# Kernel tuning notes

Measured on AMD Instinct MI355X. Metric: run time of the kernel, lower is better.

Reference implementation:

```python
import jax, jax.numpy as jnp
import numpy as np

B, C, H, W = 16, 128, 48, 48
C4 = C // 4
N = H * W
BN_EPS = 1e-5


def conv_bn_relu(x, w, gamma, beta, mean, var):
    # 1x1 conv (no bias) as channel contraction, then eval-mode BatchNorm, then ReLU
    y = jnp.einsum('bchw,oc->bohw', x, w)
    scale = gamma / jnp.sqrt(var + BN_EPS)
    y = y * scale[None, :, None, None] + (beta - mean * scale)[None, :, None, None]
    return jax.nn.relu(y)


def setup_inputs() -> dict:
    key = jax.random.key(0)
    ks = jax.random.split(key, 16)
    inp = {
        'x_en': jax.random.normal(ks[0], (B, C, H, W), dtype=jnp.float32),
        'x_de': jax.random.normal(ks[1], (B, C, H, W), dtype=jnp.float32),
        'x_cat': jax.random.normal(ks[2], (B, 2 * C, H, W), dtype=jnp.float32),
        # Get_KQ: Conv2d(C -> C/4, 1x1, no bias) + BN(C/4) (shared for K and Q)
        'w_kq': jax.random.normal(ks[3], (C4, C), dtype=jnp.float32) * 0.05,
        'kq_gamma': jax.random.normal(ks[4], (C4,), dtype=jnp.float32) * 0.1 + 1.0,
        'kq_beta': jax.random.normal(ks[5], (C4,), dtype=jnp.float32) * 0.1,
        'kq_mean': jax.random.normal(ks[6], (C4,), dtype=jnp.float32) * 0.1,
        'kq_var': jax.random.uniform(ks[7], (C4,), dtype=jnp.float32) + 0.5,
        # Get_V: Conv2d(C -> C, 1x1, no bias) + BN(C)
        'w_v': jax.random.normal(ks[8], (C, C), dtype=jnp.float32) * 0.05,
        'v_gamma': jax.random.normal(ks[9], (C,), dtype=jnp.float32) * 0.1 + 1.0,
        'v_beta': jax.random.normal(ks[10], (C,), dtype=jnp.float32) * 0.1,
        'v_mean': jax.random.normal(ks[11], (C,), dtype=jnp.float32) * 0.1,
        'v_var': jax.random.uniform(ks[12], (C,), dtype=jnp.float32) + 0.5,
        # reduce_channels: Conv2d(2C -> C, 1x1, no bias) + BN(C)
        'w_red': jax.random.normal(ks[13], (C, 2 * C), dtype=jnp.float32) * 0.05,
        'red_gamma': jax.random.normal(ks[14], (C,), dtype=jnp.float32) * 0.1 + 1.0,
        'red_beta': jax.random.normal(ks[15], (C,), dtype=jnp.float32) * 0.1,
        'red_mean': jax.random.normal(jax.random.fold_in(key, 100), (C,), dtype=jnp.float32) * 0.1,
        'red_var': jax.random.uniform(jax.random.fold_in(key, 101), (C,), dtype=jnp.float32) + 0.5,
    }
    return inp


def reference(x_en, x_de, x_cat,
              w_kq, kq_gamma, kq_beta, kq_mean, kq_var,
              w_v, v_gamma, v_beta, v_mean, v_var,
              w_red, red_gamma, red_beta, red_mean, red_var):
    Kf = conv_bn_relu(x_en, w_kq, kq_gamma, kq_beta, kq_mean, kq_var).reshape(B, C4, N)
    Qf = conv_bn_relu(x_de, w_kq, kq_gamma, kq_beta, kq_mean, kq_var).reshape(B, C4, N)
    # KQ[b, n, m] = sum_k K[b, k, n] * Q[b, k, m]  -> [B, N, N]
    KQ = jnp.einsum('bkn,bkm->bnm', Kf, Qf)
    # GLOBAL softmax over the flattened N*N map (per batch), not per row
    A = jax.nn.softmax(KQ.reshape(B, N * N), axis=1).reshape(B, N, N)
    x = conv_bn_relu(x_cat, w_red, red_gamma, red_beta, red_mean, red_var)
    V = conv_bn_relu(x, w_v, v_gamma, v_beta, v_mean, v_var).reshape(B, C, N)
    # FeatureMap[b, c, n] = sum_m V[b, c, m] * A[b, n, m]
    feat = jnp.einsum('bcm,bnm->bcn', V, A).reshape(B, C, H, W)
    return jnp.concatenate([x, feat], axis=1)
```

## Files before the change

### kernel.cpp

```cpp
#include <hip/hip_runtime.h>
#include <math.h>

#define C    128
#define C4   32
#define NN   2304
#define BN_EPS 1e-5f
#define NEG_INF -3.402823466e38f
#define LOG2E 1.4426950408889634f

typedef short bf16x8 __attribute__((ext_vector_type(8)));
typedef float f32x4 __attribute__((ext_vector_type(4)));

#define SOFT_BARRIER() asm volatile("s_waitcnt lgkmcnt(0)\n\ts_barrier" ::: "memory")

__device__ inline unsigned short f2bf(float f) {
    unsigned int u = __float_as_uint(f);
    u += 0x7fffu + ((u >> 16) & 1u);
    return (unsigned short)(u >> 16);
}

__device__ inline unsigned int pk2bf(float a, float b) {
#if __has_builtin(__builtin_amdgcn_cvt_pk_bf16_f32)
    typedef __bf16 bf2 __attribute__((ext_vector_type(2)));
    bf2 v = __builtin_amdgcn_cvt_pk_bf16_f32(a, b);
    return __builtin_bit_cast(unsigned int, v);
#else
    unsigned int ua = __float_as_uint(a); ua += 0x7fffu + ((ua >> 16) & 1u);
    unsigned int ub = __float_as_uint(b); ub += 0x7fffu + ((ub >> 16) & 1u);
    return __builtin_amdgcn_perm(ub, ua, 0x07060302u);
#endif
}

__device__ inline float fexp2(float x) {
#if __has_builtin(__builtin_amdgcn_exp2f)
    return __builtin_amdgcn_exp2f(x);
#else
    return __expf(x * 0.69314718055994531f);
#endif
}


__global__ __launch_bounds__(256) void k_wprep(
    const float* __restrict__ wkq, const float* __restrict__ kq_g,
    const float* __restrict__ kq_b, const float* __restrict__ kq_m,
    const float* __restrict__ kq_v,
    const float* __restrict__ wv, const float* __restrict__ v_g,
    const float* __restrict__ v_b, const float* __restrict__ v_m,
    const float* __restrict__ v_v,
    const float* __restrict__ wred, const float* __restrict__ red_g,
    const float* __restrict__ red_b, const float* __restrict__ red_m,
    const float* __restrict__ red_v,
    unsigned short* __restrict__ wkq_bf, unsigned short* __restrict__ wv_bf,
    unsigned short* __restrict__ wred_bf,
    float* __restrict__ kq_sh, float* __restrict__ v_sh, float* __restrict__ red_sh)
{
    const int t = blockIdx.x * 256 + threadIdx.x;
    if (t < 4096) {
        const int o = t >> 7;
        const float sc = kq_g[o] * rsqrtf(kq_v[o] + BN_EPS);
        wkq_bf[t] = f2bf(wkq[t] * sc);
        if ((t & 127) == 0) kq_sh[o] = kq_b[o] - kq_m[o] * sc;
    } else if (t < 4096 + 16384) {
        const int e = t - 4096;
        const int o = e >> 7;
        const float sc = v_g[o] * rsqrtf(v_v[o] + BN_EPS);
        wv_bf[e] = f2bf(wv[e] * sc);
        if ((e & 127) == 0) v_sh[o] = v_b[o] - v_m[o] * sc;
    } else if (t < 4096 + 16384 + 32768) {
        const int e = t - 20480;
        const int o = e >> 8;
        const float sc = red_g[o] * rsqrtf(red_v[o] + BN_EPS);
        wred_bf[e] = f2bf(wred[e] * sc);
        if ((e & 255) == 0) red_sh[o] = red_b[o] - red_m[o] * sc;
    }
}

__global__ __launch_bounds__(256) void k_kq(
    const float* __restrict__ x0, const float* __restrict__ x1,
    const unsigned short* __restrict__ wbf, const float* __restrict__ shift,
    unsigned short* __restrict__ Kt, unsigned short* __restrict__ Qt)
{
    constexpr int NTILE = 128, R = 8;
    __shared__ unsigned short Xs[NTILE][40];

    const int tid = threadIdx.x;
    const int w = tid >> 6, lane = tid & 63;
    const int quad = lane >> 4, l16 = lane & 15;
    const int b = blockIdx.y, n0 = blockIdx.x * NTILE;
    const int nbase = w * 32;

    const float* xin = (blockIdx.z ? x1 : x0) + (size_t)b * C * NN;
    const int p = tid & 15, g = tid >> 4;

    f32x4 acc[2][2];
#pragma unroll
    for (int mt = 0; mt < 2; mt++)
#pragma unroll
        for (int nt = 0; nt < 2; nt++) acc[mt][nt] = (f32x4){0.f, 0.f, 0.f, 0.f};

    for (int c0 = 0; c0 < C; c0 += 32) {
        __syncthreads();
        {
            const float* xr = xin + (size_t)(c0 + 2 * p) * NN + n0 + g * R;
            float av[R], bv[R];
#pragma unroll
            for (int i4 = 0; i4 < R; i4 += 4) {
                *(float4*)&av[i4] = *(const float4*)&xr[i4];
                *(float4*)&bv[i4] = *(const float4*)&xr[NN + i4];
            }
            unsigned int* Xw = (unsigned int*)Xs;
#pragma unroll
            for (int i = 0; i < R; i++)
                Xw[(g * R + i) * 20 + p] = pk2bf(av[i], bv[i]);
        }
        __syncthreads();
        bf16x8 af[2];
#pragma unroll
        for (int mt = 0; mt < 2; mt++)
            af[mt] = *(const bf16x8*)&wbf[(size_t)(mt * 16 + l16) * C + c0 + quad * 8];
#pragma unroll
        for (int nt = 0; nt < 2; nt++) {
            const bf16x8 bfr = *(const bf16x8*)&Xs[nbase + nt * 16 + l16][quad * 8];
#pragma unroll
            for (int mt = 0; mt < 2; mt++)
                acc[mt][nt] = __builtin_amdgcn_mfma_f32_16x16x32_bf16(af[mt], bfr, acc[mt][nt], 0, 0, 0);
        }
    }

    unsigned short* ob16 = blockIdx.z ? Qt : Kt;
    const float osc = blockIdx.z ? 1.f : LOG2E;
#pragma unroll
    for (int mt = 0; mt < 2; mt++)
#pragma unroll
        for (int nt = 0; nt < 2; nt++)
#pragma unroll
            for (int r = 0; r < 4; r++) {
                const int o = mt * 16 + quad * 4 + r;
                const int n = n0 + nbase + nt * 16 + l16;
                const float sh = shift[o];
                ob16[((size_t)b * NN + n) * 32 + o] =
                    f2bf(fmaxf(acc[mt][nt][r] + sh, 0.f) * osc);
            }
}

__global__ __launch_bounds__(256) void k_redv(
    const float* __restrict__ xcat,
    const unsigned short* __restrict__ wred_bf, const float* __restrict__ red_sh,
    const unsigned short* __restrict__ wv_bf,  const float* __restrict__ v_sh,
    float* __restrict__ out, unsigned short* __restrict__ Vf)
{
    __shared__ unsigned short Xs[48][40];
    __shared__ unsigned int   Xv[64 * 49];

    const int tid = threadIdx.x;
    const int w = tid >> 6, lane = tid & 63;
    const int quad = lane >> 4, l16 = lane & 15;
    const int b = blockIdx.y, n0 = blockIdx.x * 48;
    const float* xin = xcat + (size_t)b * 2 * C * NN;
    const int p = tid & 15, g = tid >> 4;

    f32x4 acc[2][3];
#pragma unroll
    for (int mt = 0; mt < 2; mt++)
#pragma unroll
        for (int nt = 0; nt < 3; nt++) acc[mt][nt] = (f32x4){0.f, 0.f, 0.f, 0.f};

    for (int c0 = 0; c0 < 2 * C; c0 += 32) {
        __syncthreads();
        if (g < 12) {
            const float* xr = xin + (size_t)(c0 + 2 * p) * NN + n0 + g * 4;
            float4 av = *(const float4*)&xr[0];
            float4 bv = *(const float4*)&xr[NN];
            unsigned int* Xw = (unsigned int*)Xs;
            Xw[(g * 4 + 0) * 20 + p] = pk2bf(av.x, bv.x);
            Xw[(g * 4 + 1) * 20 + p] = pk2bf(av.y, bv.y);
            Xw[(g * 4 + 2) * 20 + p] = pk2bf(av.z, bv.z);
            Xw[(g * 4 + 3) * 20 + p] = pk2bf(av.w, bv.w);
        }
        __syncthreads();
        bf16x8 af[2];
#pragma unroll
        for (int mt = 0; mt < 2; mt++)
            af[mt] = *(const bf16x8*)&wred_bf[(size_t)(w * 32 + mt * 16 + l16) * (2 * C) + c0 + quad * 8];
#pragma unroll
        for (int nt = 0; nt < 3; nt++) {
            const bf16x8 bfr = *(const bf16x8*)&Xs[nt * 16 + l16][quad * 8];
#pragma unroll
            for (int mt = 0; mt < 2; mt++)
                acc[mt][nt] = __builtin_amdgcn_mfma_f32_16x16x32_bf16(af[mt], bfr, acc[mt][nt], 0, 0, 0);
        }
    }

    {
        float* ob = out + (size_t)b * (2 * C * NN);
#pragma unroll
        for (int mt = 0; mt < 2; mt++) {
            float sh[4];
#pragma unroll
            for (int r = 0; r < 4; r++) sh[r] = red_sh[w * 32 + mt * 16 + quad * 4 + r];
#pragma unroll
            for (int nt = 0; nt < 3; nt++) {
                const int n = n0 + nt * 16 + l16;
                float v[4];
#pragma unroll
                for (int r = 0; r < 4; r++) {
                    const int o = w * 32 + mt * 16 + quad * 4 + r;
                    v[r] = fmaxf(acc[mt][nt][r] + sh[r], 0.f);
                    ob[(size_t)o * NN + n] = v[r];
                }
                const int op0 = 16 * w + mt * 8 + quad * 2;
                Xv[(op0 + 0) * 49 + nt * 16 + l16] = pk2bf(v[0], v[1]);
                Xv[(op0 + 1) * 49 + nt * 16 + l16] = pk2bf(v[2], v[3]);
            }
        }
    }
    SOFT_BARRIER();

    f32x4 vacc[2][3];
#pragma unroll
    for (int mt = 0; mt < 2; mt++)
#pragma unroll
        for (int nt = 0; nt < 3; nt++) vacc[mt][nt] = (f32x4){0.f, 0.f, 0.f, 0.f};

    for (int c0 = 0; c0 < C; c0 += 32) {
        bf16x8 af[2];
#pragma unroll
        for (int mt = 0; mt < 2; mt++)
            af[mt] = *(const bf16x8*)&wv_bf[(size_t)(w * 32 + mt * 16 + l16) * C + c0 + quad * 8];
#pragma unroll
        for (int nt = 0; nt < 3; nt++) {
            const int col = nt * 16 + l16;
            const int cp0 = c0 / 2 + quad * 4;
            uint4 u;
            u.x = Xv[(cp0 + 0) * 49 + col];
            u.y = Xv[(cp0 + 1) * 49 + col];
            u.z = Xv[(cp0 + 2) * 49 + col];
            u.w = Xv[(cp0 + 3) * 49 + col];
            const bf16x8 bfr = __builtin_bit_cast(bf16x8, u);
#pragma unroll
            for (int mt = 0; mt < 2; mt++)
                vacc[mt][nt] = __builtin_amdgcn_mfma_f32_16x16x32_bf16(af[mt], bfr, vacc[mt][nt], 0, 0, 0);
        }
    }

#pragma unroll
    for (int mt = 0; mt < 2; mt++) {
        float sh[4];
#pragma unroll
        for (int r = 0; r < 4; r++) sh[r] = v_sh[w * 32 + mt * 16 + quad * 4 + r];
#pragma unroll
        for (int nt = 0; nt < 3; nt++)
#pragma unroll
            for (int r = 0; r < 4; r++) {
                const int o = w * 32 + mt * 16 + quad * 4 + r;
                const int n = n0 + nt * 16 + l16;
                Vf[((size_t)b * C + o) * NN + n] = f2bf(fmaxf(vacc[mt][nt][r] + sh[r], 0.f));
            }
    }
}

__global__ __launch_bounds__(256) void k_stats(
    const unsigned short* __restrict__ Kt, const unsigned short* __restrict__ Qt,
    float* __restrict__ bmax, float* __restrict__ bsum)
{
    const int tid = threadIdx.x;
    const int w = tid >> 6, lane = tid & 63;
    const int quad = lane >> 4, l16 = lane & 15;
    const int b = blockIdx.z;
    const int n0 = blockIdx.x * 128, m0 = blockIdx.y * 128;
    const unsigned short* Kb = Kt + (size_t)b * NN * 32;
    const unsigned short* Qb = Qt + (size_t)b * NN * 32;

    bf16x8 kf[8], qf[2];
#pragma unroll
    for (int nt = 0; nt < 8; nt++)
        kf[nt] = *(const bf16x8*)&Kb[(size_t)(n0 + nt * 16 + l16) * 32 + quad * 8];
#pragma unroll
    for (int mt = 0; mt < 2; mt++)
        qf[mt] = *(const bf16x8*)&Qb[(size_t)(m0 + w * 32 + mt * 16 + l16) * 32 + quad * 8];

    f32x4 s[16];
#pragma unroll
    for (int mt = 0; mt < 2; mt++)
#pragma unroll
        for (int nt = 0; nt < 8; nt++) {
            f32x4 z = (f32x4){0.f, 0.f, 0.f, 0.f};
            s[mt * 8 + nt] = __builtin_amdgcn_mfma_f32_16x16x32_bf16(qf[mt], kf[nt], z, 0, 0, 0);
        }

    float lmax = NEG_INF;
#pragma unroll
    for (int i = 0; i < 16; i++)
        lmax = fmaxf(lmax, fmaxf(fmaxf(s[i][0], s[i][1]), fmaxf(s[i][2], s[i][3])));
    float lsum = 0.f;
#pragma unroll
    for (int i = 0; i < 16; i++)
        lsum += fexp2(s[i][0] - lmax) + fexp2(s[i][1] - lmax) +
                fexp2(s[i][2] - lmax) + fexp2(s[i][3] - lmax);

#pragma unroll
    for (int off = 32; off > 0; off >>= 1) {
        const float omax = __shfl_xor(lmax, off);
        const float osum = __shfl_xor(lsum, off);
        const float nmax = fmaxf(lmax, omax);
        lsum = lsum * fexp2(lmax - nmax) + osum * fexp2(omax - nmax);
        lmax = nmax;
    }
    __shared__ float smax[4], ssum[4];
    if (lane == 0) { smax[w] = lmax; ssum[w] = lsum; }
    __syncthreads();
    if (tid == 0) {
        float M = smax[0], S = ssum[0];
        for (int i = 1; i < 4; i++) {
            const float nmax = fmaxf(M, smax[i]);
            S = S * fexp2(M - nmax) + ssum[i] * fexp2(smax[i] - nmax);
            M = nmax;
        }
        const int idx = (b * 18 + blockIdx.y) * 18 + blockIdx.x;
        bmax[idx] = M;
        bsum[idx] = S;
    }
}

__global__ __launch_bounds__(256) void k_fin(
    const float* __restrict__ bmax, const float* __restrict__ bsum,
    float* __restrict__ Ms, float* __restrict__ Sinv)
{
    __shared__ float rmax[256], rsum[256];
    const int b = blockIdx.x, tid = threadIdx.x;
    float lmax = NEG_INF, lsum = 0.f;
    for (int i = tid; i < 324; i += 256) {
        const float m = bmax[b * 324 + i], s = bsum[b * 324 + i];
        const float nmax = fmaxf(lmax, m);
        lsum = lsum * fexp2(lmax - nmax) + s * fexp2(m - nmax);
        lmax = nmax;
    }
    rmax[tid] = lmax; rsum[tid] = lsum;
    __syncthreads();
    for (int st = 128; st > 0; st >>= 1) {
        if (tid < st) {
            const float m2 = rmax[tid + st], s2 = rsum[tid + st];
            const float nmax = fmaxf(rmax[tid], m2);
            rsum[tid] = rsum[tid] * fexp2(rmax[tid] - nmax) + s2 * fexp2(m2 - nmax);
            rmax[tid] = nmax;
        }
        __syncthreads();
    }
    if (tid == 0) { Ms[b] = rmax[0]; Sinv[b] = 1.f / rsum[0]; }
}

__global__ __launch_bounds__(256) void k_feat(
    const unsigned short* __restrict__ Kt, const unsigned short* __restrict__ Qt,
    const unsigned short* __restrict__ Vf, const float* __restrict__ Ms,
    const float* __restrict__ Sinv, float* __restrict__ out)
{
    __shared__ __align__(16) unsigned short Et[48][72];
    const int tid = threadIdx.x;
    const int w = tid >> 6, lane = tid & 63;
    const int quad = lane >> 4, l16 = lane & 15;
    const int b = blockIdx.y, n0 = blockIdx.x * 48;
    const unsigned short* Kb = Kt + (size_t)b * NN * 32;
    const unsigned short* Qb = Qt + (size_t)b * NN * 32;
    const unsigned short* Vb = Vf + (size_t)b * C * NN;
    const float M = Ms[b], Si = Sinv[b];

    bf16x8 kf[3];
#pragma unroll
    for (int nt = 0; nt < 3; nt++)
        kf[nt] = *(const bf16x8*)&Kb[(size_t)(n0 + nt * 16 + l16) * 32 + quad * 8];

    f32x4 acc[2][3];
#pragma unroll
    for (int i = 0; i < 2; i++)
#pragma unroll
        for (int j = 0; j < 3; j++) acc[i][j] = (f32x4){0.f, 0.f, 0.f, 0.f};

    bf16x8 qc = *(const bf16x8*)&Qb[(size_t)(w * 16 + l16) * 32 + quad * 8];
    bf16x8 vc[2][2];
#pragma unroll
    for (int ct = 0; ct < 2; ct++)
#pragma unroll
        for (int ks = 0; ks < 2; ks++)
            vc[ct][ks] = *(const bf16x8*)&Vb[(size_t)(w * 32 + ct * 16 + l16) * NN + ks * 32 + quad * 8];

    for (int m0 = 0; m0 < NN; m0 += 64) {
        f32x4 s[3];
#pragma unroll
        for (int nt = 0; nt < 3; nt++) {
            f32x4 z = (f32x4){0.f, 0.f, 0.f, 0.f};
            s[nt] = __builtin_amdgcn_mfma_f32_16x16x32_bf16(qc, kf[nt], z, 0, 0, 0);
        }
        const int m1 = (m0 + 64 < NN) ? m0 + 64 : 0;
        bf16x8 qn = *(const bf16x8*)&Qb[(size_t)(m1 + w * 16 + l16) * 32 + quad * 8];
        bf16x8 vn[2][2];
#pragma unroll
        for (int ct = 0; ct < 2; ct++)
#pragma unroll
            for (int ks = 0; ks < 2; ks++)
                vn[ct][ks] = *(const bf16x8*)&Vb[(size_t)(w * 32 + ct * 16 + l16) * NN + m1 + ks * 32 + quad * 8];

#pragma unroll
        for (int nt = 0; nt < 3; nt++) {
            const unsigned int u0 = pk2bf(fexp2(s[nt][0] - M), fexp2(s[nt][1] - M));
            const unsigned int u1 = pk2bf(fexp2(s[nt][2] - M), fexp2(s[nt][3] - M));
            *(uint2*)&Et[nt * 16 + l16][w * 16 + quad * 4] = make_uint2(u0, u1);
        }
        SOFT_BARRIER();
#pragma unroll
        for (int ks = 0; ks < 2; ks++) {
#pragma unroll
            for (int nt = 0; nt < 3; nt++) {
                const bf16x8 ef = *(const bf16x8*)&Et[nt * 16 + l16][ks * 32 + quad * 8];
                acc[0][nt] = __builtin_amdgcn_mfma_f32_16x16x32_bf16(vc[0][ks], ef, acc[0][nt], 0, 0, 0);
                acc[1][nt] = __builtin_amdgcn_mfma_f32_16x16x32_bf16(vc[1][ks], ef, acc[1][nt], 0, 0, 0);
            }
        }
        SOFT_BARRIER();
        qc = qn;
#pragma unroll
        for (int ct = 0; ct < 2; ct++)
#pragma unroll
            for (int ks = 0; ks < 2; ks++) vc[ct][ks] = vn[ct][ks];
    }

    float* ob = out + (size_t)b * 2 * C * NN + (size_t)C * NN + n0;
#pragma unroll
    for (int ct = 0; ct < 2; ct++)
#pragma unroll
        for (int nt = 0; nt < 3; nt++)
#pragma unroll
            for (int r = 0; r < 4; r++) {
                const int c = w * 32 + ct * 16 + quad * 4 + r;
                ob[(size_t)c * NN + nt * 16 + l16] = acc[ct][nt][r] * Si;
            }
}

extern "C" void kernel_launch(void* const* d_in, const int* in_sizes, int n_in,
                              void* d_out, int out_size, void* d_ws, size_t ws_size,
                              hipStream_t stream)
{
    const float* x_en   = (const float*)d_in[0];
    const float* x_de   = (const float*)d_in[1];
    const float* x_cat  = (const float*)d_in[2];
    const float* w_kq   = (const float*)d_in[3];
    const float* kq_g   = (const float*)d_in[4];
    const float* kq_b   = (const float*)d_in[5];
    const float* kq_m   = (const float*)d_in[6];
    const float* kq_v   = (const float*)d_in[7];
    const float* w_v    = (const float*)d_in[8];
    const float* v_g    = (const float*)d_in[9];
    const float* v_b    = (const float*)d_in[10];
    const float* v_m    = (const float*)d_in[11];
    const float* v_v    = (const float*)d_in[12];
    const float* w_red  = (const float*)d_in[13];
    const float* red_g  = (const float*)d_in[14];
    const float* red_b  = (const float*)d_in[15];
    const float* red_m  = (const float*)d_in[16];
    const float* red_v  = (const float*)d_in[17];

    unsigned short* Kt      = (unsigned short*)d_ws;
    unsigned short* Qt      = Kt + 1179648;
    unsigned short* Vf      = Qt + 1179648;
    unsigned short* wkq_bf  = Vf + 4718592;
    unsigned short* wv_bf   = wkq_bf + 4096;
    unsigned short* wred_bf = wv_bf + 16384;
    float* bmax = (float*)(wred_bf + 32768);
    float* bsum = bmax + 16 * 324;
    float* Ms   = bsum + 16 * 324;
    float* Sinv = Ms + 16;
    float* kq_sh  = Sinv + 16;
    float* v_sh   = kq_sh + 32;
    float* red_sh = v_sh + 128;
    float* out  = (float*)d_out;

    k_wprep<<<208, 256, 0, stream>>>(
        w_kq, kq_g, kq_b, kq_m, kq_v,
        w_v, v_g, v_b, v_m, v_v,
        w_red, red_g, red_b, red_m, red_v,
        wkq_bf, wv_bf, wred_bf, kq_sh, v_sh, red_sh);

    k_kq  <<<dim3(18, 16, 2), 256, 0, stream>>>(x_en, x_de, wkq_bf, kq_sh, Kt, Qt);
    k_redv<<<dim3(48, 16), 256, 0, stream>>>(x_cat, wred_bf, red_sh, wv_bf, v_sh, out, Vf);

    k_stats<<<dim3(18, 18, 16), 256, 0, stream>>>(Kt, Qt, bmax, bsum);
    k_fin  <<<16, 256, 0, stream>>>(bmax, bsum, Ms, Sinv);
    k_feat <<<dim3(48, 16), 256, 0, stream>>>(Kt, Qt, Vf, Ms, Sinv, out);
}
```

Baseline: 247.7 us.

## Double-buffer LDS tiles and software-pipeline loads in conv and attention kernels

The 1x1-conv kernels (k_kq, k_redv) now use two LDS buffers and prefetch the next channel slice into registers before writing the current one. This drops one barrier per iteration and overlaps global loads with MFMA work. k_feat double-buffers the exp-score tile: it computes scores and exponentials for the next 64-column chunk while the current chunk feeds the V·A MFMAs, so only one barrier per iteration remains. The cost is more LDS and register pressure, which could lower occupancy.

```diff
diff --git a/kernel.cpp b/kernel.cpp
--- a/kernel.cpp
+++ b/kernel.cpp
@@ -81,7 +81,7 @@
     unsigned short* __restrict__ Kt, unsigned short* __restrict__ Qt)
 {
     constexpr int NTILE = 128, R = 8;
-    __shared__ unsigned short Xs[NTILE][40];
+    __shared__ unsigned short Xs[2][NTILE][40];
 
     const int tid = threadIdx.x;
     const int w = tid >> 6, lane = tid & 63;
@@ -98,29 +98,41 @@
 #pragma unroll
         for (int nt = 0; nt < 2; nt++) acc[mt][nt] = (f32x4){0.f, 0.f, 0.f, 0.f};
 
-    for (int c0 = 0; c0 < C; c0 += 32) {
-        __syncthreads();
-        {
-            const float* xr = xin + (size_t)(c0 + 2 * p) * NN + n0 + g * R;
-            float av[R], bv[R];
+    const float* xrb = xin + n0 + g * R;
+    float av[R], bv[R];
+    {
+        const float* xr = xrb + (size_t)(2 * p) * NN;
+#pragma unroll
+        for (int i4 = 0; i4 < R; i4 += 4) {
+            *(float4*)&av[i4] = *(const float4*)&xr[i4];
+            *(float4*)&bv[i4] = *(const float4*)&xr[NN + i4];
+        }
+    }
+
+    for (int k = 0; k < 4; ++k) {
+        unsigned int uu[R];
+#pragma unroll
+        for (int i = 0; i < R; i++) uu[i] = pk2bf(av[i], bv[i]);
+        if (k < 3) {
+            const float* xr = xrb + (size_t)((k + 1) * 32 + 2 * p) * NN;
 #pragma unroll
             for (int i4 = 0; i4 < R; i4 += 4) {
                 *(float4*)&av[i4] = *(const float4*)&xr[i4];
                 *(float4*)&bv[i4] = *(const float4*)&xr[NN + i4];
             }
-            unsigned int* Xw = (unsigned int*)Xs;
-#pragma unroll
-            for (int i = 0; i < R; i++)
-                Xw[(g * R + i) * 20 + p] = pk2bf(av[i], bv[i]);
-        }
-        __syncthreads();
+        }
+        unsigned int* Xw = (unsigned int*)Xs[k & 1];
+#pragma unroll
+        for (int i = 0; i < R; i++)
+            Xw[(g * R + i) * 20 + p] = uu[i];
+        SOFT_BARRIER();
         bf16x8 af[2];
 #pragma unroll
         for (int mt = 0; mt < 2; mt++)
-            af[mt] = *(const bf16x8*)&wbf[(size_t)(mt * 16 + l16) * C + c0 + quad * 8];
+            af[mt] = *(const bf16x8*)&wbf[(size_t)(mt * 16 + l16) * C + k * 32 + quad * 8];
 #pragma unroll
         for (int nt = 0; nt < 2; nt++) {
-            const bf16x8 bfr = *(const bf16x8*)&Xs[nbase + nt * 16 + l16][quad * 8];
+            const bf16x8 bfr = *(const bf16x8*)&Xs[k & 1][nbase + nt * 16 + l16][quad * 8];
 #pragma unroll
             for (int mt = 0; mt < 2; mt++)
                 acc[mt][nt] = __builtin_amdgcn_mfma_f32_16x16x32_bf16(af[mt], bfr, acc[mt][nt], 0, 0, 0);
@@ -149,7 +161,7 @@
     const unsigned short* __restrict__ wv_bf,  const float* __restrict__ v_sh,
     float* __restrict__ out, unsigned short* __restrict__ Vf)
 {
-    __shared__ unsigned short Xs[48][40];
+    __shared__ unsigned short Xs[2][48][40];
     __shared__ unsigned int   Xv[64 * 49];
 
     const int tid = threadIdx.x;
@@ -165,26 +177,38 @@
 #pragma unroll
         for (int nt = 0; nt < 3; nt++) acc[mt][nt] = (f32x4){0.f, 0.f, 0.f, 0.f};
 
-    for (int c0 = 0; c0 < 2 * C; c0 += 32) {
-        __syncthreads();
+    float4 av, bv;
+    if (g < 12) {
+        const float* xr = xin + (size_t)(2 * p) * NN + n0 + g * 4;
+        av = *(const float4*)&xr[0];
+        bv = *(const float4*)&xr[NN];
+    }
+
+    for (int k = 0; k < 8; ++k) {
         if (g < 12) {
-            const float* xr = xin + (size_t)(c0 + 2 * p) * NN + n0 + g * 4;
-            float4 av = *(const float4*)&xr[0];
-            float4 bv = *(const float4*)&xr[NN];
-            unsigned int* Xw = (unsigned int*)Xs;
-            Xw[(g * 4 + 0) * 20 + p] = pk2bf(av.x, bv.x);
-            Xw[(g * 4 + 1) * 20 + p] = pk2bf(av.y, bv.y);
-            Xw[(g * 4 + 2) * 20 + p] = pk2bf(av.z, bv.z);
-            Xw[(g * 4 + 3) * 20 + p] = pk2bf(av.w, bv.w);
-        }
-        __syncthreads();
+            const unsigned int u0 = pk2bf(av.x, bv.x);
+            const unsigned int u1 = pk2bf(av.y, bv.y);
+            const unsigned int u2 = pk2bf(av.z, bv.z);
+            const unsigned int u3 = pk2bf(av.w, bv.w);
+            if (k < 7) {
+                const float* xr = xin + (size_t)((k + 1) * 32 + 2 * p) * NN + n0 + g * 4;
+                av = *(const float4*)&xr[0];
+                bv = *(const float4*)&xr[NN];
+            }
+            unsigned int* Xw = (unsigned int*)Xs[k & 1];
+            Xw[(g * 4 + 0) * 20 + p] = u0;
+            Xw[(g * 4 + 1) * 20 + p] = u1;
+            Xw[(g * 4 + 2) * 20 + p] = u2;
+            Xw[(g * 4 + 3) * 20 + p] = u3;
+        }
+        SOFT_BARRIER();
         bf16x8 af[2];
 #pragma unroll
         for (int mt = 0; mt < 2; mt++)
-            af[mt] = *(const bf16x8*)&wred_bf[(size_t)(w * 32 + mt * 16 + l16) * (2 * C) + c0 + quad * 8];
+            af[mt] = *(const bf16x8*)&wred_bf[(size_t)(w * 32 + mt * 16 + l16) * (2 * C) + k * 32 + quad * 8];
 #pragma unroll
         for (int nt = 0; nt < 3; nt++) {
-            const bf16x8 bfr = *(const bf16x8*)&Xs[nt * 16 + l16][quad * 8];
+            const bf16x8 bfr = *(const bf16x8*)&Xs[k & 1][nt * 16 + l16][quad * 8];
 #pragma unroll
             for (int mt = 0; mt < 2; mt++)
                 acc[mt][nt] = __builtin_amdgcn_mfma_f32_16x16x32_bf16(af[mt], bfr, acc[mt][nt], 0, 0, 0);
@@ -354,7 +378,7 @@
     const unsigned short* __restrict__ Vf, const float* __restrict__ Ms,
     const float* __restrict__ Sinv, float* __restrict__ out)
 {
-    __shared__ __align__(16) unsigned short Et[48][72];
+    __shared__ __align__(16) unsigned short Et[2][48][72];
     const int tid = threadIdx.x;
     const int w = tid >> 6, lane = tid & 63;
     const int quad = lane >> 4, l16 = lane & 15;
@@ -375,42 +399,62 @@
 #pragma unroll
         for (int j = 0; j < 3; j++) acc[i][j] = (f32x4){0.f, 0.f, 0.f, 0.f};
 
-    bf16x8 qc = *(const bf16x8*)&Qb[(size_t)(w * 16 + l16) * 32 + quad * 8];
+    bf16x8 q0 = *(const bf16x8*)&Qb[(size_t)(w * 16 + l16) * 32 + quad * 8];
     bf16x8 vc[2][2];
 #pragma unroll
     for (int ct = 0; ct < 2; ct++)
 #pragma unroll
         for (int ks = 0; ks < 2; ks++)
             vc[ct][ks] = *(const bf16x8*)&Vb[(size_t)(w * 32 + ct * 16 + l16) * NN + ks * 32 + quad * 8];
-
-    for (int m0 = 0; m0 < NN; m0 += 64) {
-        f32x4 s[3];
+    bf16x8 qc = *(const bf16x8*)&Qb[(size_t)(64 + w * 16 + l16) * 32 + quad * 8];
+    {
+        f32x4 s0[3];
 #pragma unroll
         for (int nt = 0; nt < 3; nt++) {
             f32x4 z = (f32x4){0.f, 0.f, 0.f, 0.f};
-            s[nt] = __builtin_amdgcn_mfma_f32_16x16x32_bf16(qc, kf[nt], z, 0, 0, 0);
-        }
-        const int m1 = (m0 + 64 < NN) ? m0 + 64 : 0;
-        bf16x8 qn = *(const bf16x8*)&Qb[(size_t)(m1 + w * 16 + l16) * 32 + quad * 8];
+            s0[nt] = __builtin_amdgcn_mfma_f32_16x16x32_bf16(q0, kf[nt], z, 0, 0, 0);
+        }
+#pragma unroll
+        for (int nt = 0; nt < 3; nt++) {
+            const unsigned int u0 = pk2bf(fexp2(s0[nt][0] - M), fexp2(s0[nt][1] - M));
+            const unsigned int u1 = pk2bf(fexp2(s0[nt][2] - M), fexp2(s0[nt][3] - M));
+            *(uint2*)&Et[0][nt * 16 + l16][w * 16 + quad * 4] = make_uint2(u0, u1);
+        }
+    }
+    SOFT_BARRIER();
+
+    for (int k = 0; k < 36; ++k) {
+        const int cur = k & 1;
+        const int mq = (k + 2 < 36 ? k + 2 : 0) * 64;
+        const int mv = (k + 1 < 36 ? k + 1 : 0) * 64;
+        bf16x8 qn = *(const bf16x8*)&Qb[(size_t)(mq + w * 16 + l16) * 32 + quad * 8];
         bf16x8 vn[2][2];
 #pragma unroll
         for (int ct = 0; ct < 2; ct++)
 #pragma unroll
             for (int ks = 0; ks < 2; ks++)
-                vn[ct][ks] = *(const bf16x8*)&Vb[(size_t)(w * 32 + ct * 16 + l16) * NN + m1 + ks * 32 + quad * 8];
-
-#pragma unroll
-        for (int nt = 0; nt < 3; nt++) {
-            const unsigned int u0 = pk2bf(fexp2(s[nt][0] - M), fexp2(s[nt][1] - M));
-            const unsigned int u1 = pk2bf(fexp2(s[nt][2] - M), fexp2(s[nt][3] - M));
-            *(uint2*)&Et[nt * 16 + l16][w * 16 + quad * 4] = make_uint2(u0, u1);
-        }
-        SOFT_BARRIER();
+                vn[ct][ks] = *(const bf16x8*)&Vb[(size_t)(w * 32 + ct * 16 + l16) * NN + mv + ks * 32 + quad * 8];
+
+        if (k < 35) {
+            f32x4 s[3];
+#pragma unroll
+            for (int nt = 0; nt < 3; nt++) {
+                f32x4 z = (f32x4){0.f, 0.f, 0.f, 0.f};
+                s[nt] = __builtin_amdgcn_mfma_f32_16x16x32_bf16(qc, kf[nt], z, 0, 0, 0);
+            }
+#pragma unroll
+            for (int nt = 0; nt < 3; nt++) {
+                const unsigned int u0 = pk2bf(fexp2(s[nt][0] - M), fexp2(s[nt][1] - M));
+                const unsigned int u1 = pk2bf(fexp2(s[nt][2] - M), fexp2(s[nt][3] - M));
+                *(uint2*)&Et[cur ^ 1][nt * 16 + l16][w * 16 + quad * 4] = make_uint2(u0, u1);
+            }
+        }
+
 #pragma unroll
         for (int ks = 0; ks < 2; ks++) {
 #pragma unroll
             for (int nt = 0; nt < 3; nt++) {
-                const bf16x8 ef = *(const bf16x8*)&Et[nt * 16 + l16][ks * 32 + quad * 8];
+                const bf16x8 ef = *(const bf16x8*)&Et[cur][nt * 16 + l16][ks * 32 + quad * 8];
                 acc[0][nt] = __builtin_amdgcn_mfma_f32_16x16x32_bf16(vc[0][ks], ef, acc[0][nt], 0, 0, 0);
                 acc[1][nt] = __builtin_amdgcn_mfma_f32_16x16x32_bf16(vc[1][ks], ef, acc[1][nt], 0, 0, 0);
             }
```

Result: no change. 244.6 us (-1.3%).
